# Optimization experiments

Hardware: AMD Instinct MI355X
Metric: run time of the kernel (lower is better)

Reference implementation:

```python
import jax, jax.numpy as jnp
import numpy as np

NUM_HEADS = 16


def setup_inputs() -> dict:
    key = jax.random.key(0)
    k1, k2, k3, k4 = jax.random.split(key, 4)
    B, N, C = 4, 2048, 1024
    x = jax.random.normal(k1, (B, N, C), dtype=jnp.float32)
    # xavier-uniform-ish scaling for stable softmax
    Wqkv = jax.random.normal(k2, (C, 3 * C), dtype=jnp.float32) * (2.0 / (C + 3 * C)) ** 0.5
    Wproj = jax.random.normal(k3, (C, C), dtype=jnp.float32) * (1.0 / C) ** 0.5
    bproj = jnp.zeros((C,), dtype=jnp.float32)
    mask = jax.random.randint(k4, (B, N), 0, 2, dtype=jnp.int32)  # >0 means masked
    return {"x": x, "Wqkv": Wqkv, "Wproj": Wproj, "bproj": bproj, "mask": mask}


def reference(x, Wqkv, Wproj, bproj, mask):
    B, N, C = x.shape
    H = NUM_HEADS
    Dh = C // H
    scale = Dh ** -0.5
    qkv = x @ Wqkv                                   # [B, N, 3C]
    qkv = qkv.reshape(B, N, 3, H, Dh).transpose(2, 0, 3, 1, 4)  # [3, B, H, N, Dh]
    q, k, v = qkv[0], qkv[1], qkv[2]
    att = jnp.einsum('bhqd,bhkd->bhqk', q, k) * scale  # [B, H, N, N]
    att = jnp.where(mask[:, None, None, :] > 0, jnp.float32(-10000000.0), att)
    att = jax.nn.softmax(att, axis=-1)
    out = jnp.einsum('bhqk,bhkd->bhqd', att, v)      # [B, H, N, Dh]
    out = out.transpose(0, 2, 1, 3).reshape(B, N, C)
    return out @ Wproj + bproj
```

## Files before the change

kernel.cpp:

```cpp
#include <hip/hip_runtime.h>
#include <hip/hip_bf16.h>
#include <cstdint>

typedef __bf16 bf16x8 __attribute__((ext_vector_type(8)));
typedef float f32x4 __attribute__((ext_vector_type(4)));
typedef uint4 __attribute__((may_alias)) uint4a;

typedef __attribute__((address_space(3))) unsigned int   lds_u32;
typedef __attribute__((address_space(1))) const unsigned int gbl_u32;

#define BATCH 4
#define SEQ   2048
#define CDIM  1024
#define NH    16
#define HD    64

#define C1SCALE 0.18033688011112042f

__device__ __forceinline__ unsigned short f2bf(float f) {
    uint32_t u = __builtin_bit_cast(uint32_t, f);
    u += 0x7fffu + ((u >> 16) & 1u);
    return (unsigned short)(u >> 16);
}

#if __has_builtin(__builtin_amdgcn_cvt_pk_bf16_f32)
typedef __bf16 bf16x2 __attribute__((ext_vector_type(2)));
__device__ __forceinline__ uint32_t pk2bf(float a, float b) {
    bf16x2 v = __builtin_amdgcn_cvt_pk_bf16_f32(a, b);
    return __builtin_bit_cast(uint32_t, v);
}
#else
__device__ __forceinline__ uint32_t pk2bf(float a, float b) {
    return (uint32_t)f2bf(a) | ((uint32_t)f2bf(b) << 16);
}
#endif

__device__ __forceinline__ void g2l16(const unsigned short* g, unsigned short* l) {
    __builtin_amdgcn_global_load_lds((gbl_u32*)g, (lds_u32*)l, 16, 0, 0);
}

#define NB_CVT   8192
#define NB_TQKV  3072
#define NB_TPROJ 1024
#define NB_PREP  (NB_CVT + NB_TQKV + NB_TPROJ + 4)

__global__ __launch_bounds__(256)
void prep_kernel(const float* __restrict__ x,
                 const float* __restrict__ Wqkv,
                 const float* __restrict__ Wproj,
                 const int* __restrict__ mask,
                 unsigned short* __restrict__ xb,
                 unsigned short* __restrict__ Wqkvt,
                 unsigned short* __restrict__ Wprojt,
                 int* __restrict__ ridx, int* __restrict__ cnt) {
    __shared__ float tile[32][33];
    __shared__ int s[256];
    int bid = blockIdx.x, tid = threadIdx.x;

    if (bid < NB_CVT) {
        int i = (bid * 256 + tid) * 4;
        float4 v = *(const float4*)(x + i);
        uint2 o;
        o.x = pk2bf(v.x, v.y);
        o.y = pk2bf(v.z, v.w);
        *(uint2*)(xb + i) = o;
        return;
    }
    if (bid < NB_CVT + NB_TQKV + NB_TPROJ) {
        const float* in;
        unsigned short* out;
        int Cc, bx;
        if (bid < NB_CVT + NB_TQKV) {
            bx = bid - NB_CVT; in = Wqkv; out = Wqkvt; Cc = 3072;
        } else {
            bx = bid - NB_CVT - NB_TQKV; in = Wproj; out = Wprojt; Cc = 1024;
        }
        int nbx = Cc >> 5;
        int c0 = (bx % nbx) * 32, r0 = (bx / nbx) * 32;
        int tx = tid & 31, ty = tid >> 5;
        #pragma unroll
        for (int i = 0; i < 32; i += 8)
            tile[ty + i][tx] = in[(size_t)(r0 + ty + i) * Cc + c0 + tx];
        __syncthreads();
        #pragma unroll
        for (int i = 0; i < 32; i += 8)
            out[(size_t)(c0 + ty + i) * 1024 + r0 + tx] = f2bf(tile[tx][ty + i]);
        return;
    }
    int b = bid - (NB_CVT + NB_TQKV + NB_TPROJ);
    int keep[8], lc = 0;
    #pragma unroll
    for (int u = 0; u < 8; ++u) {
        keep[u] = (mask[b * SEQ + tid * 8 + u] > 0) ? 0 : 1;
        lc += keep[u];
    }
    s[tid] = lc;
    __syncthreads();
    for (int d = 1; d < 256; d <<= 1) {
        int w = (tid >= d) ? s[tid - d] : 0;
        __syncthreads();
        s[tid] += w;
        __syncthreads();
    }
    int pos = s[tid] - lc;
    #pragma unroll
    for (int u = 0; u < 8; ++u) {
        if (keep[u]) ridx[b * SEQ + pos++] = tid * 8 + u;
    }
    int total = s[255];
    for (int i = total + tid; i < SEQ; i += 256)
        ridx[b * SEQ + i] = 0;
    if (tid == 255) cnt[b] = total;
}

#define BK 64

__global__ __launch_bounds__(256, 2)
void gemm_q_kernel(const unsigned short* __restrict__ A,
                   const unsigned short* __restrict__ Bt,
                   unsigned short* __restrict__ Q) {
    __shared__ __align__(16) unsigned short sA[128 * 64];
    __shared__ __align__(16) unsigned short sB[128 * 64];
    const int Kdim = 1024;
    int m0 = blockIdx.x * 128;
    int n0 = blockIdx.y * 128;
    int tid = threadIdx.x;
    int wave = tid >> 6, lane = tid & 63;
    int wm = (wave >> 1) * 64, wn = (wave & 1) * 64;
    int l15 = lane & 15, quad = lane >> 4;
    int lr = lane >> 3, lc8 = ((lane & 7) ^ lr) * 8;

    f32x4 acc[4][4] = {};

    for (int k0 = 0; k0 < Kdim; k0 += BK) {
        #pragma unroll
        for (int it = 0; it < 4; ++it) {
            int c = wave * 4 + it;
            int gr = c * 8 + lr;
            g2l16(A  + (size_t)(m0 + gr) * Kdim + k0 + lc8, &sA[c * 512]);
            g2l16(Bt + (size_t)(n0 + gr) * Kdim + k0 + lc8, &sB[c * 512]);
        }
        __syncthreads();
        #pragma unroll
        for (int kk = 0; kk < BK; kk += 32) {
            bf16x8 af[4], bfr[4];
            #pragma unroll
            for (int i = 0; i < 4; ++i) {
                int r = wm + i * 16 + l15;
                int q = ((kk >> 3) + quad) ^ (r & 7);
                af[i] = __builtin_bit_cast(bf16x8, *(const uint4a*)(&sA[r * 64 + q * 8]));
            }
            #pragma unroll
            for (int j = 0; j < 4; ++j) {
                int r = wn + j * 16 + l15;
                int q = ((kk >> 3) + quad) ^ (r & 7);
                bfr[j] = __builtin_bit_cast(bf16x8, *(const uint4a*)(&sB[r * 64 + q * 8]));
            }
            #pragma unroll
            for (int i = 0; i < 4; ++i)
                #pragma unroll
                for (int j = 0; j < 4; ++j)
                    acc[i][j] = __builtin_amdgcn_mfma_f32_16x16x32_bf16(af[i], bfr[j], acc[i][j], 0, 0, 0);
        }
        __syncthreads();
    }

    #pragma unroll
    for (int i = 0; i < 4; ++i) {
        #pragma unroll
        for (int j = 0; j < 4; ++j) {
            int col = n0 + wn + j * 16 + l15;
            int h = col >> 6;
            int d = col & 63;
            int row0 = m0 + wm + i * 16 + quad * 4;
            int b = row0 >> 11, n = row0 & 2047;
            size_t bh = (size_t)(b * NH + h);
            uint32_t p01 = pk2bf(acc[i][j][0] * C1SCALE, acc[i][j][1] * C1SCALE);
            uint32_t p23 = pk2bf(acc[i][j][2] * C1SCALE, acc[i][j][3] * C1SCALE);
            size_t base = (bh * SEQ + n) * HD + d;
            Q[base]          = (unsigned short)p01;
            Q[base + HD]     = (unsigned short)(p01 >> 16);
            Q[base + 2 * HD] = (unsigned short)p23;
            Q[base + 3 * HD] = (unsigned short)(p23 >> 16);
        }
    }
}

__global__ __launch_bounds__(256, 2)
void gemm_kv_kernel(const unsigned short* __restrict__ A,
                    const unsigned short* __restrict__ Bt,
                    const int* __restrict__ ridx,
                    const int* __restrict__ cnt,
                    unsigned short* __restrict__ Kc,
                    unsigned short* __restrict__ Vct) {
    __shared__ __align__(16) unsigned short sA[128 * 64];
    __shared__ __align__(16) unsigned short sB[128 * 64];
    const int Kdim = 1024;
    int b  = blockIdx.x >> 4;
    int m0 = (blockIdx.x & 15) * 128;
    const int kn = cnt[b];
    if (m0 >= kn) return;
    int n0 = 1024 + blockIdx.y * 128;
    int tid = threadIdx.x;
    int wave = tid >> 6, lane = tid & 63;
    int wm = (wave >> 1) * 64, wn = (wave & 1) * 64;
    int l15 = lane & 15, quad = lane >> 4;
    int lr = lane >> 3, lc8 = ((lane & 7) ^ lr) * 8;

    const unsigned short* aRow[4];
    #pragma unroll
    for (int it = 0; it < 4; ++it) {
        int gr = (wave * 4 + it) * 8 + lr;
        int rid = ridx[b * SEQ + m0 + gr];
        aRow[it] = A + (size_t)(b * SEQ + rid) * Kdim + lc8;
    }

    f32x4 acc[4][4] = {};

    for (int k0 = 0; k0 < Kdim; k0 += BK) {
        #pragma unroll
        for (int it = 0; it < 4; ++it) {
            int c = wave * 4 + it;
            int gr = c * 8 + lr;
            g2l16(aRow[it] + k0, &sA[c * 512]);
            g2l16(Bt + (size_t)(n0 + gr) * Kdim + k0 + lc8, &sB[c * 512]);
        }
        __syncthreads();
        #pragma unroll
        for (int kk = 0; kk < BK; kk += 32) {
            bf16x8 af[4], bfr[4];
            #pragma unroll
            for (int i = 0; i < 4; ++i) {
                int r = wm + i * 16 + l15;
                int q = ((kk >> 3) + quad) ^ (r & 7);
                af[i] = __builtin_bit_cast(bf16x8, *(const uint4a*)(&sA[r * 64 + q * 8]));
            }
            #pragma unroll
            for (int j = 0; j < 4; ++j) {
                int r = wn + j * 16 + l15;
                int q = ((kk >> 3) + quad) ^ (r & 7);
                bfr[j] = __builtin_bit_cast(bf16x8, *(const uint4a*)(&sB[r * 64 + q * 8]));
            }
            #pragma unroll
            for (int i = 0; i < 4; ++i)
                #pragma unroll
                for (int j = 0; j < 4; ++j)
                    acc[i][j] = __builtin_amdgcn_mfma_f32_16x16x32_bf16(af[i], bfr[j], acc[i][j], 0, 0, 0);
        }
        __syncthreads();
    }

    #pragma unroll
    for (int i = 0; i < 4; ++i) {
        #pragma unroll
        for (int j = 0; j < 4; ++j) {
            int c2 = (n0 - 1024) + wn + j * 16 + l15;
            int three = c2 >> 10;
            int h = (c2 >> 6) & 15;
            int d = c2 & 63;
            int pf0 = m0 + wm + i * 16 + quad * 4;
            size_t bh = (size_t)(b * NH + h);
            if (three == 0) {
                #pragma unroll
                for (int r = 0; r < 4; ++r) {
                    int pf = pf0 + r;
                    if (pf < kn) Kc[(bh * SEQ + pf) * HD + d] = f2bf(acc[i][j][r]);
                }
            } else {
                #pragma unroll
                for (int r = 0; r < 4; ++r) {
                    int pf = pf0 + r;
                    if (pf < kn) Vct[(bh * HD + d) * SEQ + pf] = f2bf(acc[i][j][r]);
                }
            }
        }
    }
}

__global__ __launch_bounds__(256, 2)
void gemm_proj_kernel(const unsigned short* __restrict__ A,
                      const unsigned short* __restrict__ Bt,
                      const float* __restrict__ bias,
                      float* __restrict__ Out) {
    __shared__ __align__(16) unsigned short sA[128 * 64];
    __shared__ __align__(16) unsigned short sB[128 * 64];
    const int Kdim = 1024;
    int m0 = blockIdx.x * 128;
    int n0 = blockIdx.y * 128;
    int tid = threadIdx.x;
    int wave = tid >> 6, lane = tid & 63;
    int wm = (wave >> 1) * 64, wn = (wave & 1) * 64;
    int l15 = lane & 15, quad = lane >> 4;
    int lr = lane >> 3, lc8 = ((lane & 7) ^ lr) * 8;

    f32x4 acc[4][4] = {};

    for (int k0 = 0; k0 < Kdim; k0 += BK) {
        #pragma unroll
        for (int it = 0; it < 4; ++it) {
            int c = wave * 4 + it;
            int gr = c * 8 + lr;
            g2l16(A  + (size_t)(m0 + gr) * Kdim + k0 + lc8, &sA[c * 512]);
            g2l16(Bt + (size_t)(n0 + gr) * Kdim + k0 + lc8, &sB[c * 512]);
        }
        __syncthreads();
        #pragma unroll
        for (int kk = 0; kk < BK; kk += 32) {
            bf16x8 af[4], bfr[4];
            #pragma unroll
            for (int i = 0; i < 4; ++i) {
                int r = wm + i * 16 + l15;
                int q = ((kk >> 3) + quad) ^ (r & 7);
                af[i] = __builtin_bit_cast(bf16x8, *(const uint4a*)(&sA[r * 64 + q * 8]));
            }
            #pragma unroll
            for (int j = 0; j < 4; ++j) {
                int r = wn + j * 16 + l15;
                int q = ((kk >> 3) + quad) ^ (r & 7);
                bfr[j] = __builtin_bit_cast(bf16x8, *(const uint4a*)(&sB[r * 64 + q * 8]));
            }
            #pragma unroll
            for (int i = 0; i < 4; ++i)
                #pragma unroll
                for (int j = 0; j < 4; ++j)
                    acc[i][j] = __builtin_amdgcn_mfma_f32_16x16x32_bf16(af[i], bfr[j], acc[i][j], 0, 0, 0);
        }
        __syncthreads();
    }

    #pragma unroll
    for (int i = 0; i < 4; ++i) {
        #pragma unroll
        for (int j = 0; j < 4; ++j) {
            int col = n0 + wn + j * 16 + l15;
            float bv = bias[col];
            #pragma unroll
            for (int r = 0; r < 4; ++r) {
                int row = m0 + wm + i * 16 + quad * 4 + r;
                Out[(size_t)row * CDIM + col] = acc[i][j][r] + bv;
            }
        }
    }
}

#define SPD 72

__global__ __launch_bounds__(256, 4)
void flash_attn_kernel(const unsigned short* __restrict__ Q,
                       const unsigned short* __restrict__ Kg,
                       const unsigned short* __restrict__ Vt,
                       const int* __restrict__ cnt,
                       unsigned short* __restrict__ O) {
    int bh = blockIdx.x;
    int q0 = blockIdx.y * 128;
    int b = bh >> 4, h = bh & 15;
    int tid = threadIdx.x;
    int wave = tid >> 6, lane = tid & 63;
    int l15 = lane & 15, quad = lane >> 4;
    int lr = lane >> 3, lc8 = ((lane & 7) ^ lr) * 8;

    const int kn = cnt[b];

    const size_t head_off = (size_t)bh * SEQ * HD;
    const unsigned short* Qh = Q + head_off;
    const unsigned short* Kh = Kg + head_off;
    const unsigned short* Vh = Vt + head_off;

    __shared__ __align__(16) unsigned short sK [64 * 64];
    __shared__ __align__(16) unsigned short sVt[64 * 64];
    __shared__ __align__(16) unsigned short sP [4][16 * SPD];

    bf16x8 qf[2][2];
    #pragma unroll
    for (int mt = 0; mt < 2; ++mt) {
        const unsigned short* qp = Qh + (size_t)(q0 + wave * 32 + mt * 16 + l15) * HD + quad * 8;
        qf[mt][0] = __builtin_bit_cast(bf16x8, *(const uint4a*)(qp));
        qf[mt][1] = __builtin_bit_cast(bf16x8, *(const uint4a*)(qp + 32));
    }

    bf16x8 ones;
    {
        uint4 ov;
        ov.x = ov.y = ov.z = ov.w = 0x3F803F80u;
        ones = __builtin_bit_cast(bf16x8, ov);
    }

    f32x4 oacc[2][4] = {};
    f32x4 oextra[2] = {};

    for (int k0 = 0; k0 < kn; k0 += 64) {
        #pragma unroll
        for (int it = 0; it < 2; ++it) {
            int c = wave * 2 + it;
            int gr = c * 8 + lr;
            g2l16(Kh + (size_t)(k0 + gr) * HD + lc8, &sK[c * 512]);
            g2l16(Vh + (size_t)gr * SEQ + k0 + lc8, &sVt[c * 512]);
        }
        __syncthreads();

        bool tail = (k0 + 64 > kn);

        #pragma unroll
        for (int mt = 0; mt < 2; ++mt) {
            f32x4 s[4] = {};
            #pragma unroll
            for (int j = 0; j < 4; ++j) {
                int r = j * 16 + l15, sw = r & 7;
                uint4 v0 = *(const uint4a*)(&sK[r * 64 + ((quad ^ sw) * 8)]);
                uint4 v1 = *(const uint4a*)(&sK[r * 64 + (((4 + quad) ^ sw) * 8)]);
                __builtin_amdgcn_s_setprio(1);
                s[j] = __builtin_amdgcn_mfma_f32_16x16x32_bf16(qf[mt][0], __builtin_bit_cast(bf16x8, v0), s[j], 0, 0, 0);
                s[j] = __builtin_amdgcn_mfma_f32_16x16x32_bf16(qf[mt][1], __builtin_bit_cast(bf16x8, v1), s[j], 0, 0, 0);
                __builtin_amdgcn_s_setprio(0);
            }
            unsigned short* sp = &sP[wave][0];
            if (tail) {
                #pragma unroll
                for (int j = 0; j < 4; ++j) {
                    float madd = (k0 + j * 16 + l15 < kn) ? 0.f : -1e30f;
                    #pragma unroll
                    for (int r = 0; r < 4; ++r)
                        s[j][r] = __builtin_amdgcn_exp2f(s[j][r] + madd);
                }
            } else {
                #pragma unroll
                for (int j = 0; j < 4; ++j)
                    #pragma unroll
                    for (int r = 0; r < 4; ++r)
                        s[j][r] = __builtin_amdgcn_exp2f(s[j][r]);
            }
            #pragma unroll
            for (int j = 0; j < 4; ++j) {
                uint32_t p01 = pk2bf(s[j][0], s[j][1]);
                uint32_t p23 = pk2bf(s[j][2], s[j][3]);
                int base = quad * 4 * SPD + j * 16 + l15;
                sp[base]           = (unsigned short)p01;
                sp[base + SPD]     = (unsigned short)(p01 >> 16);
                sp[base + 2 * SPD] = (unsigned short)p23;
                sp[base + 3 * SPD] = (unsigned short)(p23 >> 16);
            }
            #pragma unroll
            for (int kc = 0; kc < 2; ++kc) {
                uint4 av = *(const uint4a*)(&sp[l15 * SPD + kc * 32 + quad * 8]);
                bf16x8 af = __builtin_bit_cast(bf16x8, av);
                __builtin_amdgcn_s_setprio(1);
                #pragma unroll
                for (int jd = 0; jd < 4; ++jd) {
                    int r = jd * 16 + l15;
                    int q = ((kc * 4 + quad) ^ (r & 7)) * 8;
                    uint4 bv = *(const uint4a*)(&sVt[r * 64 + q]);
                    oacc[mt][jd] = __builtin_amdgcn_mfma_f32_16x16x32_bf16(af, __builtin_bit_cast(bf16x8, bv), oacc[mt][jd], 0, 0, 0);
                }
                oextra[mt] = __builtin_amdgcn_mfma_f32_16x16x32_bf16(af, ones, oextra[mt], 0, 0, 0);
                __builtin_amdgcn_s_setprio(0);
            }
        }
        __syncthreads();
    }

    #pragma unroll
    for (int mt = 0; mt < 2; ++mt) {
        float rl[4];
        #pragma unroll
        for (int r = 0; r < 4; ++r) rl[r] = __builtin_amdgcn_rcpf(oextra[mt][r]);
        #pragma unroll
        for (int jd = 0; jd < 4; ++jd) {
            int d = jd * 16 + l15;
            size_t base = ((size_t)(b * SEQ + q0 + wave * 32 + mt * 16 + quad * 4)) * CDIM + h * HD + d;
            uint32_t p01 = pk2bf(oacc[mt][jd][0] * rl[0], oacc[mt][jd][1] * rl[1]);
            uint32_t p23 = pk2bf(oacc[mt][jd][2] * rl[2], oacc[mt][jd][3] * rl[3]);
            O[base]            = (unsigned short)p01;
            O[base + CDIM]     = (unsigned short)(p01 >> 16);
            O[base + 2 * CDIM] = (unsigned short)p23;
            O[base + 3 * CDIM] = (unsigned short)(p23 >> 16);
        }
    }
}

extern "C" void kernel_launch(void* const* d_in, const int* in_sizes, int n_in,
                              void* d_out, int out_size, void* d_ws, size_t ws_size,
                              hipStream_t stream) {
    const float* x     = (const float*)d_in[0];
    const float* Wqkv  = (const float*)d_in[1];
    const float* Wproj = (const float*)d_in[2];
    const float* bproj = (const float*)d_in[3];
    const int*   mask  = (const int*)d_in[4];
    float* out = (float*)d_out;

    char* ws = (char*)d_ws;
    unsigned short* xb     = (unsigned short*)(ws);
    unsigned short* Wqkvt  = (unsigned short*)(ws + (16u << 20));
    unsigned short* Wprojt = (unsigned short*)(ws + (22u << 20));
    unsigned short* Qb     = (unsigned short*)(ws + (24u << 20));
    unsigned short* Kb     = (unsigned short*)(ws + (40u << 20));
    unsigned short* Vtb    = (unsigned short*)(ws + (56u << 20));
    int*            ridx   = (int*)(ws + (72u << 20));
    int*            cntb   = (int*)(ws + (72u << 20) + (32u << 10));

    prep_kernel<<<dim3(NB_PREP), dim3(256), 0, stream>>>(x, Wqkv, Wproj, mask,
                                                         xb, Wqkvt, Wprojt, ridx, cntb);
    gemm_q_kernel<<<dim3(64, 8), dim3(256), 0, stream>>>(xb, Wqkvt, Qb);
    gemm_kv_kernel<<<dim3(64, 16), dim3(256), 0, stream>>>(xb, Wqkvt, ridx, cntb, Kb, Vtb);
    flash_attn_kernel<<<dim3(64, 16), dim3(256), 0, stream>>>(Qb, Kb, Vtb, cntb, xb);
    gemm_proj_kernel<<<dim3(64, 8), dim3(256), 0, stream>>>(xb, Wprojt, bproj, out);
}
```

Measured before the change: 238.8 us.

## Merge Q and KV projection GEMMs into one launch; batch both row tiles in attention

The separate Q and K/V projection kernels become one kernel with a 24-column grid that branches on blockIdx.y, so Q tiles and compacted K/V tiles run in a single launch. This removes one kernel launch and the tail gap between the two GEMMs. In the attention kernel, QK scores for both 16-row sub-tiles are computed together, both P tiles are written to a larger shared buffer, and the PV MFMAs for both sub-tiles share each V fragment load. This adds register and LDS pressure in exchange for fewer repeated K and V shared-memory reads and more independent MFMAs.

```diff
diff --git a/kernel.cpp b/kernel.cpp
--- a/kernel.cpp
+++ b/kernel.cpp
@@ -116,20 +116,48 @@
 #define BK 64
 
 __global__ __launch_bounds__(256, 2)
-void gemm_q_kernel(const unsigned short* __restrict__ A,
-                   const unsigned short* __restrict__ Bt,
-                   unsigned short* __restrict__ Q) {
+void gemm_qkv2_kernel(const unsigned short* __restrict__ A,
+                      const unsigned short* __restrict__ Bt,
+                      const int* __restrict__ ridx,
+                      const int* __restrict__ cnt,
+                      unsigned short* __restrict__ Q,
+                      unsigned short* __restrict__ Kc,
+                      unsigned short* __restrict__ Vct) {
     __shared__ __align__(16) unsigned short sA[128 * 64];
     __shared__ __align__(16) unsigned short sB[128 * 64];
     const int Kdim = 1024;
-    int m0 = blockIdx.x * 128;
-    int n0 = blockIdx.y * 128;
     int tid = threadIdx.x;
     int wave = tid >> 6, lane = tid & 63;
     int wm = (wave >> 1) * 64, wn = (wave & 1) * 64;
     int l15 = lane & 15, quad = lane >> 4;
     int lr = lane >> 3, lc8 = ((lane & 7) ^ lr) * 8;
 
+    const bool qpath = (blockIdx.y < 8);
+    int m0, n0, b = 0, kn = 0;
+    const unsigned short* aPtr[4];
+
+    if (qpath) {
+        m0 = blockIdx.x * 128;
+        n0 = blockIdx.y * 128;
+        #pragma unroll
+        for (int it = 0; it < 4; ++it) {
+            int gr = (wave * 4 + it) * 8 + lr;
+            aPtr[it] = A + (size_t)(m0 + gr) * Kdim + lc8;
+        }
+    } else {
+        b  = blockIdx.x >> 4;
+        m0 = (blockIdx.x & 15) * 128;
+        kn = cnt[b];
+        if (m0 >= kn) return;
+        n0 = 1024 + (blockIdx.y - 8) * 128;
+        #pragma unroll
+        for (int it = 0; it < 4; ++it) {
+            int gr = (wave * 4 + it) * 8 + lr;
+            int rid = ridx[b * SEQ + m0 + gr];
+            aPtr[it] = A + (size_t)(b * SEQ + rid) * Kdim + lc8;
+        }
+    }
+
     f32x4 acc[4][4] = {};
 
     for (int k0 = 0; k0 < Kdim; k0 += BK) {
@@ -137,7 +165,7 @@
         for (int it = 0; it < 4; ++it) {
             int c = wave * 4 + it;
             int gr = c * 8 + lr;
-            g2l16(A  + (size_t)(m0 + gr) * Kdim + k0 + lc8, &sA[c * 512]);
+            g2l16(aPtr[it] + k0, &sA[c * 512]);
             g2l16(Bt + (size_t)(n0 + gr) * Kdim + k0 + lc8, &sB[c * 512]);
         }
         __syncthreads();
@@ -165,112 +193,49 @@
         __syncthreads();
     }
 
-    #pragma unroll
-    for (int i = 0; i < 4; ++i) {
-        #pragma unroll
-        for (int j = 0; j < 4; ++j) {
-            int col = n0 + wn + j * 16 + l15;
-            int h = col >> 6;
-            int d = col & 63;
-            int row0 = m0 + wm + i * 16 + quad * 4;
-            int b = row0 >> 11, n = row0 & 2047;
-            size_t bh = (size_t)(b * NH + h);
-            uint32_t p01 = pk2bf(acc[i][j][0] * C1SCALE, acc[i][j][1] * C1SCALE);
-            uint32_t p23 = pk2bf(acc[i][j][2] * C1SCALE, acc[i][j][3] * C1SCALE);
-            size_t base = (bh * SEQ + n) * HD + d;
-            Q[base]          = (unsigned short)p01;
-            Q[base + HD]     = (unsigned short)(p01 >> 16);
-            Q[base + 2 * HD] = (unsigned short)p23;
-            Q[base + 3 * HD] = (unsigned short)(p23 >> 16);
-        }
-    }
-}
-
-__global__ __launch_bounds__(256, 2)
-void gemm_kv_kernel(const unsigned short* __restrict__ A,
-                    const unsigned short* __restrict__ Bt,
-                    const int* __restrict__ ridx,
-                    const int* __restrict__ cnt,
-                    unsigned short* __restrict__ Kc,
-                    unsigned short* __restrict__ Vct) {
-    __shared__ __align__(16) unsigned short sA[128 * 64];
-    __shared__ __align__(16) unsigned short sB[128 * 64];
-    const int Kdim = 1024;
-    int b  = blockIdx.x >> 4;
-    int m0 = (blockIdx.x & 15) * 128;
-    const int kn = cnt[b];
-    if (m0 >= kn) return;
-    int n0 = 1024 + blockIdx.y * 128;
-    int tid = threadIdx.x;
-    int wave = tid >> 6, lane = tid & 63;
-    int wm = (wave >> 1) * 64, wn = (wave & 1) * 64;
-    int l15 = lane & 15, quad = lane >> 4;
-    int lr = lane >> 3, lc8 = ((lane & 7) ^ lr) * 8;
-
-    const unsigned short* aRow[4];
-    #pragma unroll
-    for (int it = 0; it < 4; ++it) {
-        int gr = (wave * 4 + it) * 8 + lr;
-        int rid = ridx[b * SEQ + m0 + gr];
-        aRow[it] = A + (size_t)(b * SEQ + rid) * Kdim + lc8;
-    }
-
-    f32x4 acc[4][4] = {};
-
-    for (int k0 = 0; k0 < Kdim; k0 += BK) {
-        #pragma unroll
-        for (int it = 0; it < 4; ++it) {
-            int c = wave * 4 + it;
-            int gr = c * 8 + lr;
-            g2l16(aRow[it] + k0, &sA[c * 512]);
-            g2l16(Bt + (size_t)(n0 + gr) * Kdim + k0 + lc8, &sB[c * 512]);
-        }
-        __syncthreads();
-        #pragma unroll
-        for (int kk = 0; kk < BK; kk += 32) {
-            bf16x8 af[4], bfr[4];
-            #pragma unroll
-            for (int i = 0; i < 4; ++i) {
-                int r = wm + i * 16 + l15;
-                int q = ((kk >> 3) + quad) ^ (r & 7);
-                af[i] = __builtin_bit_cast(bf16x8, *(const uint4a*)(&sA[r * 64 + q * 8]));
-            }
+    if (qpath) {
+        #pragma unroll
+        for (int i = 0; i < 4; ++i) {
             #pragma unroll
             for (int j = 0; j < 4; ++j) {
-                int r = wn + j * 16 + l15;
-                int q = ((kk >> 3) + quad) ^ (r & 7);
-                bfr[j] = __builtin_bit_cast(bf16x8, *(const uint4a*)(&sB[r * 64 + q * 8]));
-            }
-            #pragma unroll
-            for (int i = 0; i < 4; ++i)
-                #pragma unroll
-                for (int j = 0; j < 4; ++j)
-                    acc[i][j] = __builtin_amdgcn_mfma_f32_16x16x32_bf16(af[i], bfr[j], acc[i][j], 0, 0, 0);
-        }
-        __syncthreads();
-    }
-
-    #pragma unroll
-    for (int i = 0; i < 4; ++i) {
-        #pragma unroll
-        for (int j = 0; j < 4; ++j) {
-            int c2 = (n0 - 1024) + wn + j * 16 + l15;
-            int three = c2 >> 10;
-            int h = (c2 >> 6) & 15;
-            int d = c2 & 63;
-            int pf0 = m0 + wm + i * 16 + quad * 4;
-            size_t bh = (size_t)(b * NH + h);
-            if (three == 0) {
-                #pragma unroll
-                for (int r = 0; r < 4; ++r) {
-                    int pf = pf0 + r;
-                    if (pf < kn) Kc[(bh * SEQ + pf) * HD + d] = f2bf(acc[i][j][r]);
-                }
-            } else {
-                #pragma unroll
-                for (int r = 0; r < 4; ++r) {
-                    int pf = pf0 + r;
-                    if (pf < kn) Vct[(bh * HD + d) * SEQ + pf] = f2bf(acc[i][j][r]);
+                int col = n0 + wn + j * 16 + l15;
+                int h = col >> 6;
+                int d = col & 63;
+                int row0 = m0 + wm + i * 16 + quad * 4;
+                int bb = row0 >> 11, n = row0 & 2047;
+                size_t bh = (size_t)(bb * NH + h);
+                uint32_t p01 = pk2bf(acc[i][j][0] * C1SCALE, acc[i][j][1] * C1SCALE);
+                uint32_t p23 = pk2bf(acc[i][j][2] * C1SCALE, acc[i][j][3] * C1SCALE);
+                size_t base = (bh * SEQ + n) * HD + d;
+                Q[base]          = (unsigned short)p01;
+                Q[base + HD]     = (unsigned short)(p01 >> 16);
+                Q[base + 2 * HD] = (unsigned short)p23;
+                Q[base + 3 * HD] = (unsigned short)(p23 >> 16);
+            }
+        }
+    } else {
+        #pragma unroll
+        for (int i = 0; i < 4; ++i) {
+            #pragma unroll
+            for (int j = 0; j < 4; ++j) {
+                int c2 = (n0 - 1024) + wn + j * 16 + l15;
+                int three = c2 >> 10;
+                int h = (c2 >> 6) & 15;
+                int d = c2 & 63;
+                int pf0 = m0 + wm + i * 16 + quad * 4;
+                size_t bh = (size_t)(b * NH + h);
+                if (three == 0) {
+                    #pragma unroll
+                    for (int r = 0; r < 4; ++r) {
+                        int pf = pf0 + r;
+                        if (pf < kn) Kc[(bh * SEQ + pf) * HD + d] = f2bf(acc[i][j][r]);
+                    }
+                } else {
+                    #pragma unroll
+                    for (int r = 0; r < 4; ++r) {
+                        int pf = pf0 + r;
+                        if (pf < kn) Vct[(bh * HD + d) * SEQ + pf] = f2bf(acc[i][j][r]);
+                    }
                 }
             }
         }
@@ -368,7 +333,7 @@
 
     __shared__ __align__(16) unsigned short sK [64 * 64];
     __shared__ __align__(16) unsigned short sVt[64 * 64];
-    __shared__ __align__(16) unsigned short sP [4][16 * SPD];
+    __shared__ __align__(16) unsigned short sP [4][32 * SPD];
 
     bf16x8 qf[2][2];
     #pragma unroll
@@ -400,60 +365,71 @@
 
         bool tail = (k0 + 64 > kn);
 
+        f32x4 s[2][4] = {};
+        #pragma unroll
+        for (int j = 0; j < 4; ++j) {
+            int r = j * 16 + l15, sw = r & 7;
+            uint4 v0 = *(const uint4a*)(&sK[r * 64 + ((quad ^ sw) * 8)]);
+            uint4 v1 = *(const uint4a*)(&sK[r * 64 + (((4 + quad) ^ sw) * 8)]);
+            bf16x8 k0f = __builtin_bit_cast(bf16x8, v0);
+            bf16x8 k1f = __builtin_bit_cast(bf16x8, v1);
+            __builtin_amdgcn_s_setprio(1);
+            s[0][j] = __builtin_amdgcn_mfma_f32_16x16x32_bf16(qf[0][0], k0f, s[0][j], 0, 0, 0);
+            s[0][j] = __builtin_amdgcn_mfma_f32_16x16x32_bf16(qf[0][1], k1f, s[0][j], 0, 0, 0);
+            s[1][j] = __builtin_amdgcn_mfma_f32_16x16x32_bf16(qf[1][0], k0f, s[1][j], 0, 0, 0);
+            s[1][j] = __builtin_amdgcn_mfma_f32_16x16x32_bf16(qf[1][1], k1f, s[1][j], 0, 0, 0);
+            __builtin_amdgcn_s_setprio(0);
+        }
+
+        unsigned short* sp = &sP[wave][0];
         #pragma unroll
         for (int mt = 0; mt < 2; ++mt) {
-            f32x4 s[4] = {};
-            #pragma unroll
-            for (int j = 0; j < 4; ++j) {
-                int r = j * 16 + l15, sw = r & 7;
-                uint4 v0 = *(const uint4a*)(&sK[r * 64 + ((quad ^ sw) * 8)]);
-                uint4 v1 = *(const uint4a*)(&sK[r * 64 + (((4 + quad) ^ sw) * 8)]);
-                __builtin_amdgcn_s_setprio(1);
-                s[j] = __builtin_amdgcn_mfma_f32_16x16x32_bf16(qf[mt][0], __builtin_bit_cast(bf16x8, v0), s[j], 0, 0, 0);
-                s[j] = __builtin_amdgcn_mfma_f32_16x16x32_bf16(qf[mt][1], __builtin_bit_cast(bf16x8, v1), s[j], 0, 0, 0);
-                __builtin_amdgcn_s_setprio(0);
-            }
-            unsigned short* sp = &sP[wave][0];
             if (tail) {
                 #pragma unroll
                 for (int j = 0; j < 4; ++j) {
                     float madd = (k0 + j * 16 + l15 < kn) ? 0.f : -1e30f;
                     #pragma unroll
                     for (int r = 0; r < 4; ++r)
-                        s[j][r] = __builtin_amdgcn_exp2f(s[j][r] + madd);
+                        s[mt][j][r] = __builtin_amdgcn_exp2f(s[mt][j][r] + madd);
                 }
             } else {
                 #pragma unroll
                 for (int j = 0; j < 4; ++j)
                     #pragma unroll
                     for (int r = 0; r < 4; ++r)
-                        s[j][r] = __builtin_amdgcn_exp2f(s[j][r]);
+                        s[mt][j][r] = __builtin_amdgcn_exp2f(s[mt][j][r]);
             }
             #pragma unroll
             for (int j = 0; j < 4; ++j) {
-                uint32_t p01 = pk2bf(s[j][0], s[j][1]);
-                uint32_t p23 = pk2bf(s[j][2], s[j][3]);
-                int base = quad * 4 * SPD + j * 16 + l15;
+                uint32_t p01 = pk2bf(s[mt][j][0], s[mt][j][1]);
+                uint32_t p23 = pk2bf(s[mt][j][2], s[mt][j][3]);
+                int base = (mt * 16 + quad * 4) * SPD + j * 16 + l15;
                 sp[base]           = (unsigned short)p01;
                 sp[base + SPD]     = (unsigned short)(p01 >> 16);
                 sp[base + 2 * SPD] = (unsigned short)p23;
                 sp[base + 3 * SPD] = (unsigned short)(p23 >> 16);
             }
-            #pragma unroll
-            for (int kc = 0; kc < 2; ++kc) {
-                uint4 av = *(const uint4a*)(&sp[l15 * SPD + kc * 32 + quad * 8]);
-                bf16x8 af = __builtin_bit_cast(bf16x8, av);
-                __builtin_amdgcn_s_setprio(1);
-                #pragma unroll
-                for (int jd = 0; jd < 4; ++jd) {
-                    int r = jd * 16 + l15;
-                    int q = ((kc * 4 + quad) ^ (r & 7)) * 8;
-                    uint4 bv = *(const uint4a*)(&sVt[r * 64 + q]);
-                    oacc[mt][jd] = __builtin_amdgcn_mfma_f32_16x16x32_bf16(af, __builtin_bit_cast(bf16x8, bv), oacc[mt][jd], 0, 0, 0);
-                }
-                oextra[mt] = __builtin_amdgcn_mfma_f32_16x16x32_bf16(af, ones, oextra[mt], 0, 0, 0);
-                __builtin_amdgcn_s_setprio(0);
-            }
+        }
+
+        #pragma unroll
+        for (int kc = 0; kc < 2; ++kc) {
+            uint4 a0 = *(const uint4a*)(&sp[(l15)      * SPD + kc * 32 + quad * 8]);
+            uint4 a1 = *(const uint4a*)(&sp[(16 + l15) * SPD + kc * 32 + quad * 8]);
+            bf16x8 af0 = __builtin_bit_cast(bf16x8, a0);
+            bf16x8 af1 = __builtin_bit_cast(bf16x8, a1);
+            __builtin_amdgcn_s_setprio(1);
+            #pragma unroll
+            for (int jd = 0; jd < 4; ++jd) {
+                int r = jd * 16 + l15;
+                int q = ((kc * 4 + quad) ^ (r & 7)) * 8;
+                uint4 bv = *(const uint4a*)(&sVt[r * 64 + q]);
+                bf16x8 vf = __builtin_bit_cast(bf16x8, bv);
+                oacc[0][jd] = __builtin_amdgcn_mfma_f32_16x16x32_bf16(af0, vf, oacc[0][jd], 0, 0, 0);
+                oacc[1][jd] = __builtin_amdgcn_mfma_f32_16x16x32_bf16(af1, vf, oacc[1][jd], 0, 0, 0);
+            }
+            oextra[0] = __builtin_amdgcn_mfma_f32_16x16x32_bf16(af0, ones, oextra[0], 0, 0, 0);
+            oextra[1] = __builtin_amdgcn_mfma_f32_16x16x32_bf16(af1, ones, oextra[1], 0, 0, 0);
+            __builtin_amdgcn_s_setprio(0);
         }
         __syncthreads();
     }
@@ -499,8 +475,7 @@
 
     prep_kernel<<<dim3(NB_PREP), dim3(256), 0, stream>>>(x, Wqkv, Wproj, mask,
                                                          xb, Wqkvt, Wprojt, ridx, cntb);
-    gemm_q_kernel<<<dim3(64, 8), dim3(256), 0, stream>>>(xb, Wqkvt, Qb);
-    gemm_kv_kernel<<<dim3(64, 16), dim3(256), 0, stream>>>(xb, Wqkvt, ridx, cntb, Kb, Vtb);
+    gemm_qkv2_kernel<<<dim3(64, 24), dim3(256), 0, stream>>>(xb, Wqkvt, ridx, cntb, Qb, Kb, Vtb);
     flash_attn_kernel<<<dim3(64, 16), dim3(256), 0, stream>>>(Qb, Kb, Vtb, cntb, xb);
     gemm_proj_kernel<<<dim3(64, 8), dim3(256), 0, stream>>>(xb, Wprojt, bproj, out);
 }
```

Measured after the change: 227.5 us. -4.8%, faster.
